# Performance work log

Hardware: AMD Instinct MI355X
Metric: run time of the kernel (lower is better)

Reference implementation:

```python
import jax, jax.numpy as jnp
import numpy as np

OUT_PLANES = 32
IN_PLANES = 16
PROD_DW = 256                      # prod_dw_in_planes
REP = PROD_DW // IN_PLANES         # 16
# group_list: deepcopy([4,4]); append(in_planes); reverse -> [16, 4, 4]
GROUP_LIST = [IN_PLANES, 4, 4]
B, H, W = 8, 32, 32


def setup_inputs() -> dict:
    key = jax.random.key(0)
    k1, k2, k3 = jax.random.split(key, 3)
    x = jax.random.normal(k1, (B, PROD_DW, H, W), dtype=jnp.float32)
    x2 = jax.random.normal(k2, (B, IN_PLANES, H, W), dtype=jnp.float32)
    # kaiming_normal_ on (512,1,1,1): fan_in = 1 -> std = sqrt(2)
    pw_weight = jax.random.normal(k3, (OUT_PLANES * IN_PLANES, 1, 1, 1), dtype=jnp.float32) * np.float32(np.sqrt(2.0))
    return {"x": x, "x2": x2, "pw_weight": pw_weight}


def reference(x, x2, pw_weight):
    b, c, h, w = x.shape
    w2 = pw_weight.reshape(OUT_PLANES, IN_PLANES)  # (o, i)
    # Grouped 1x1 conv with 1 channel per group == elementwise multiply.
    # Flattened channel order of out1 is (out, in, rep): weight index o*i repeated
    # REP times, input channel = (in*REP + r) = x channel g % PROD_DW.
    x4 = x.reshape(b, 1, IN_PLANES, REP, h, w)
    out1 = (x4 * w2[None, :, :, None, None, None]).reshape(b, OUT_PLANES * PROD_DW, h, w)
    # segment-sum over groups of IN_PLANES consecutive channels, then threshold gate
    summed_out1 = out1.reshape(b, -1, IN_PLANES, h, w).sum(axis=2)
    flag = (summed_out1 > 0).astype(out1.dtype)
    out1 = out1 * jnp.repeat(flag, IN_PLANES, axis=1)
    # hierarchical segment sums down to out_planes channels (check path in original)
    r = out1
    for g in GROUP_LIST:
        r = r.reshape(b, -1, g, h, w).sum(axis=2)
    relu_summed_out1 = r  # computed as in original (used only for the printed check)
    # dense 1x1 conv path
    out2 = jnp.einsum('bihw,oi->bohw', x2, w2)
    relu_out2 = jax.nn.relu(out2)
    return (out1, relu_out2)
```

## Files before the change

### kernel.cpp

```cpp
#include <hip/hip_runtime.h>

typedef float f4 __attribute__((ext_vector_type(4)));

constexpr int OUTP = 32;
constexpr int INP  = 16;
constexpr int REPS = 16;
constexpr int BB   = 8;
constexpr int HW   = 32 * 32;
constexpr int P4   = HW / 4;
constexpr size_t OUT1_F4 = (size_t)BB * OUTP * INP * REPS * P4;

__global__ __launch_bounds__(1024) void qconv_pw_fused(
    const f4* __restrict__ x,
    const f4* __restrict__ x2,
    const float* __restrict__ w,
    f4* __restrict__ out)
{
    __shared__ f4 lds[REPS][64];

    const int blk = blockIdx.x;
    const int tid = threadIdx.x;

    if (blk < 512) {
        const int chunk = blk & 3;
        const int bi    = blk >> 2;
        const int b     = bi >> 4;
        const int i     = bi & 15;
        const int r     = tid >> 6;
        const int lane  = tid & 63;
        const int v     = chunk * 64 + lane;

        const f4 xv = x[(size_t)(b * 256 + i * REPS + r) * P4 + v];

        lds[r][lane] = xv;
        __syncthreads();
        f4 S = xv;
#pragma unroll
        for (int k = 8; k >= 1; k >>= 1) {
            if (r < k) { S += lds[r + k][lane]; lds[r][lane] = S; }
            __syncthreads();
        }
        S = lds[0][lane];

        const size_t base0 = (size_t)(((b * OUTP) * INP + i) * REPS + r) * P4 + v;
#pragma unroll
        for (int o = 0; o < OUTP; ++o) {
            const float wo = w[o * INP + i];
            f4 res;
            res.x = (wo * S.x > 0.f) ? xv.x * wo : 0.f;
            res.y = (wo * S.y > 0.f) ? xv.y * wo : 0.f;
            res.z = (wo * S.z > 0.f) ? xv.z * wo : 0.f;
            res.w = (wo * S.w > 0.f) ? xv.w * wo : 0.f;
            out[base0 + (size_t)o * (INP * REPS * P4)] = res;
        }
    } else {
        const int t    = (blk - 512) * 1024 + tid;
        const int v    = t & (P4 - 1);
        const int rest = t >> 8;
        const int o    = rest & (OUTP - 1);
        const int b    = rest >> 5;

        const f4* xb = x2 + (size_t)(b * INP) * P4 + v;
        f4 acc = (f4)(0.f);
#pragma unroll
        for (int i = 0; i < INP; ++i) {
            const float wo = w[o * INP + i];
            acc += xb[(size_t)i * P4] * wo;
        }
        acc.x = fmaxf(acc.x, 0.f);
        acc.y = fmaxf(acc.y, 0.f);
        acc.z = fmaxf(acc.z, 0.f);
        acc.w = fmaxf(acc.w, 0.f);

        out[OUT1_F4 + (size_t)(b * OUTP + o) * P4 + v] = acc;
    }
}

extern "C" void kernel_launch(void* const* d_in, const int* in_sizes, int n_in,
                              void* d_out, int out_size, void* d_ws, size_t ws_size,
                              hipStream_t stream) {
    const f4* x  = (const f4*)d_in[0];
    const f4* x2 = (const f4*)d_in[1];
    const float* w = (const float*)d_in[2];
    f4* out = (f4*)d_out;

    const int grid = 512 + 64;
    qconv_pw_fused<<<grid, 1024, 0, stream>>>(x, x2, w, out);
}
```

Measured before the change: 272.1 us.

## Remap work so each thread sums all reps in registers, drop LDS reduction

The out1 work is remapped so that each 256-thread block owns one (batch, out, in) slice and each thread loads all 16 rep values into registers. The segment sum is then computed in registers with no shared memory or barriers, and 16 contiguous f4 stores follow. Outputs use nontemporal stores to avoid cache pollution, and the pointwise path runs first in smaller blocks. The cost is that x is re-read once per output channel (32x redundant reads, likely served by cache), and the register footprint per thread is higher.

```diff
diff --git a/kernel.cpp b/kernel.cpp
--- a/kernel.cpp
+++ b/kernel.cpp
@@ -10,51 +10,17 @@
 constexpr int P4   = HW / 4;
 constexpr size_t OUT1_F4 = (size_t)BB * OUTP * INP * REPS * P4;
 
-__global__ __launch_bounds__(1024) void qconv_pw_fused(
+__global__ __launch_bounds__(256, 4) void qconv_pw_fused(
     const f4* __restrict__ x,
     const f4* __restrict__ x2,
     const float* __restrict__ w,
     f4* __restrict__ out)
 {
-    __shared__ f4 lds[REPS][64];
-
     const int blk = blockIdx.x;
     const int tid = threadIdx.x;
 
-    if (blk < 512) {
-        const int chunk = blk & 3;
-        const int bi    = blk >> 2;
-        const int b     = bi >> 4;
-        const int i     = bi & 15;
-        const int r     = tid >> 6;
-        const int lane  = tid & 63;
-        const int v     = chunk * 64 + lane;
-
-        const f4 xv = x[(size_t)(b * 256 + i * REPS + r) * P4 + v];
-
-        lds[r][lane] = xv;
-        __syncthreads();
-        f4 S = xv;
-#pragma unroll
-        for (int k = 8; k >= 1; k >>= 1) {
-            if (r < k) { S += lds[r + k][lane]; lds[r][lane] = S; }
-            __syncthreads();
-        }
-        S = lds[0][lane];
-
-        const size_t base0 = (size_t)(((b * OUTP) * INP + i) * REPS + r) * P4 + v;
-#pragma unroll
-        for (int o = 0; o < OUTP; ++o) {
-            const float wo = w[o * INP + i];
-            f4 res;
-            res.x = (wo * S.x > 0.f) ? xv.x * wo : 0.f;
-            res.y = (wo * S.y > 0.f) ? xv.y * wo : 0.f;
-            res.z = (wo * S.z > 0.f) ? xv.z * wo : 0.f;
-            res.w = (wo * S.w > 0.f) ? xv.w * wo : 0.f;
-            out[base0 + (size_t)o * (INP * REPS * P4)] = res;
-        }
-    } else {
-        const int t    = (blk - 512) * 1024 + tid;
+    if (blk < 256) {
+        const int t    = blk * 256 + tid;
         const int v    = t & (P4 - 1);
         const int rest = t >> 8;
         const int o    = rest & (OUTP - 1);
@@ -72,7 +38,38 @@
         acc.z = fmaxf(acc.z, 0.f);
         acc.w = fmaxf(acc.w, 0.f);
 
-        out[OUT1_F4 + (size_t)(b * OUTP + o) * P4 + v] = acc;
+        __builtin_nontemporal_store(acc, out + OUT1_F4 + (size_t)(b * OUTP + o) * P4 + v);
+    } else {
+        const int s = blk - 256;
+        const int b = s >> 9;
+        const int o = (s >> 4) & (OUTP - 1);
+        const int i = s & (INP - 1);
+        const int v = tid;
+
+        const float wo = w[o * INP + i];
+
+        const f4* xs = x + (size_t)(b * 256 + i * REPS) * P4 + v;
+        f4 xr[16];
+#pragma unroll
+        for (int r = 0; r < REPS; ++r) xr[r] = xs[(size_t)r * P4];
+
+        const f4 t0 = (xr[0] + xr[8])  + (xr[4] + xr[12]);
+        const f4 t2 = (xr[2] + xr[10]) + (xr[6] + xr[14]);
+        const f4 t1 = (xr[1] + xr[9])  + (xr[5] + xr[13]);
+        const f4 t3 = (xr[3] + xr[11]) + (xr[7] + xr[15]);
+        const f4 S  = (t0 + t2) + (t1 + t3);
+
+        f4* dst = out + (size_t)s * (REPS * P4) + v;
+#pragma unroll
+        for (int r = 0; r < REPS; ++r) {
+            const f4 xv = xr[r];
+            f4 res;
+            res.x = (wo * S.x > 0.f) ? xv.x * wo : 0.f;
+            res.y = (wo * S.y > 0.f) ? xv.y * wo : 0.f;
+            res.z = (wo * S.z > 0.f) ? xv.z * wo : 0.f;
+            res.w = (wo * S.w > 0.f) ? xv.w * wo : 0.f;
+            __builtin_nontemporal_store(res, dst + (size_t)r * P4);
+        }
     }
 }
 
@@ -84,6 +81,6 @@
     const float* w = (const float*)d_in[2];
     f4* out = (f4*)d_out;
 
-    const int grid = 512 + 64;
-    qconv_pw_fused<<<grid, 1024, 0, stream>>>(x, x2, w, out);
+    const int grid = 256 + BB * OUTP * INP;
+    qconv_pw_fused<<<grid, 256, 0, stream>>>(x, x2, w, out);
 }
```

After: 276.1 us, median of 2. No clear change (+1.5%).
